# Kernel tuning notes

Hardware: AMD Instinct MI355X
Metric: run time of the kernel (lower is better)

## Reference

```python
import jax, jax.numpy as jnp
import numpy as np
from jax import lax

EPS = 1e-5


def _bn(x, gamma, beta, mean, var):
    # x: [B,C,H,W]; params: [C]
    inv = gamma / jnp.sqrt(var + EPS)
    return x * inv[None, :, None, None] + (beta - mean * inv)[None, :, None, None]


def _conv1x1(x, w):
    # w: [O, C] pointwise conv
    return jnp.einsum('oc,bchw->bohw', w, x)


def setup_inputs() -> dict:
    dim, num_heads = 256, 8
    B, H, W = 4, 40, 40
    key = jax.random.key(0)
    ks = jax.random.split(key, 12)
    inp = {
        'x': jax.random.normal(ks[0], (B, dim, H, W), jnp.float32),
        # qkv: Conv(dim, 2*dim, k=1) = conv1x1 (no bias) + BN + SiLU
        'qkv_w': jax.random.normal(ks[1], (2 * dim, dim), jnp.float32) * 0.05,
        'qkv_gamma': jax.random.uniform(ks[2], (2 * dim,), jnp.float32, 0.5, 1.5),
        'qkv_beta': jax.random.normal(ks[3], (2 * dim,), jnp.float32) * 0.05,
        'qkv_mean': jax.random.normal(ks[4], (2 * dim,), jnp.float32) * 0.05,
        'qkv_var': jax.random.uniform(ks[5], (2 * dim,), jnp.float32, 0.5, 1.5),
        # proj: Conv(dim, dim, k=1)
        'proj_w': jax.random.normal(ks[6], (dim, dim), jnp.float32) * 0.05,
        'proj_gamma': jax.random.uniform(ks[7], (dim,), jnp.float32, 0.5, 1.5),
        'proj_beta': jax.random.normal(ks[8], (dim,), jnp.float32) * 0.05,
        'proj_mean': jax.random.normal(ks[9], (dim,), jnp.float32) * 0.05,
        'proj_var': jax.random.uniform(ks[10], (dim,), jnp.float32, 0.5, 1.5),
        # pe: depthwise 3x3 conv (groups=dim, no bias) + BN (no activation)
        'pe_w': jax.random.normal(ks[11], (dim, 1, 3, 3), jnp.float32) * 0.1,
        'pe_gamma': jax.random.uniform(jax.random.fold_in(key, 100), (dim,), jnp.float32, 0.5, 1.5),
        'pe_beta': jax.random.normal(jax.random.fold_in(key, 101), (dim,), jnp.float32) * 0.05,
        'pe_mean': jax.random.normal(jax.random.fold_in(key, 102), (dim,), jnp.float32) * 0.05,
        'pe_var': jax.random.uniform(jax.random.fold_in(key, 103), (dim,), jnp.float32, 0.5, 1.5),
    }
    return inp


def reference(x, qkv_w, qkv_gamma, qkv_beta, qkv_mean, qkv_var,
              proj_w, proj_gamma, proj_beta, proj_mean, proj_var,
              pe_w, pe_gamma, pe_beta, pe_mean, pe_var):
    B, C, H, W = x.shape
    num_heads = 8
    head_dim = C // num_heads
    N = H * W

    # positional encoding: depthwise 3x3 conv + BN
    pe = lax.conv_general_dilated(
        x, pe_w, window_strides=(1, 1), padding='SAME',
        feature_group_count=C, dimension_numbers=('NCHW', 'OIHW', 'NCHW'))
    pe = _bn(pe, pe_gamma, pe_beta, pe_mean, pe_var)

    # qkv: 1x1 conv + BN + SiLU, then split into q, k along channels
    qkv = jax.nn.silu(_bn(_conv1x1(x, qkv_w), qkv_gamma, qkv_beta, qkv_mean, qkv_var))
    q, k = qkv[:, :C], qkv[:, C:]
    v = x + pe

    # reshape to heads: q,v -> [B,h,N,d]; k -> [B,h,d,N]
    q = q.reshape(B, num_heads, head_dim, N).transpose(0, 1, 3, 2)
    k = k.reshape(B, num_heads, head_dim, N)
    v = v.reshape(B, num_heads, head_dim, N).transpose(0, 1, 3, 2)

    scale = head_dim ** (-0.5)
    attn = jnp.einsum('bhnd,bhdm->bhnm', q, k) * scale  # [B,h,N,N]
    attn = jax.nn.softmax(attn, axis=-1)
    out = jnp.einsum('bhnm,bhmd->bhnd', attn, v)        # [B,h,N,d]
    out = out.transpose(0, 1, 3, 2).reshape(B, C, H, W)

    # proj: 1x1 conv + BN + SiLU
    return jax.nn.silu(_bn(_conv1x1(out, proj_w), proj_gamma, proj_beta, proj_mean, proj_var))
```

## Files before the change

### kernel.cpp

```cpp
#include <hip/hip_runtime.h>
#include <hip/hip_bf16.h>

typedef __attribute__((ext_vector_type(8))) short short8;
typedef __attribute__((ext_vector_type(4))) float f32x4;

__device__ __forceinline__ unsigned short f2bf(float f){
    union { float f; unsigned u; } uf; uf.f = f;
    unsigned u = uf.u;
    u += 0x7FFFu + ((u >> 16) & 1u);
    return (unsigned short)(u >> 16);
}
__device__ __forceinline__ int pack2(float a, float b){
    union { float f; unsigned u; } ua, ub; ua.f = a; ub.f = b;
    unsigned x = ua.u; x += 0x7FFFu + ((x >> 16) & 1u);
    unsigned y = ub.u; y += 0x7FFFu + ((y >> 16) & 1u);
    return (int)((x >> 16) | (y & 0xFFFF0000u));
}
__device__ __forceinline__ unsigned cvtpk(float lo, float hi){
    unsigned r;
    asm("v_cvt_pk_bf16_f32 %0, %1, %2" : "=v"(r) : "v"(lo), "v"(hi));
    return r;
}
__device__ __forceinline__ float fexp2(float x){
    return __builtin_amdgcn_exp2f(x);
}

#define N_SPATIAL 1600
#define QSCALE_LOG2E 0.25506601f
#define LSTR 40

__global__ __launch_bounds__(256) void k_head2(const float* __restrict__ x,
                                               const float* __restrict__ pw,
                                               const float* __restrict__ pg,
                                               const float* __restrict__ pb,
                                               const float* __restrict__ pm,
                                               const float* __restrict__ pv,
                                               unsigned short* __restrict__ x_t,
                                               unsigned short* __restrict__ v_mf){
    __shared__ float xs[32][163];
    int pbi = blockIdx.x;
    int b = pbi/200, h=(pbi/25)%8, kt=pbi%25;
    int t = threadIdx.x;
    int winStart = kt*64 - 48;
    const float* xbase = x + ((size_t)(b*256 + h*32))*N_SPATIAL;
    #pragma unroll
    for (int i=0;i<20;i++){
        int idx = t + i*256;
        int row = idx / 160, col = idx - row*160;
        int n = winStart + col;
        float val = ((unsigned)n < 1600u) ? xbase[(size_t)row*N_SPATIAL + n] : 0.f;
        xs[row][col] = val;
    }
    __syncthreads();

    {
        unsigned short* xtb = x_t + ((size_t)b*N_SPATIAL + kt*64)*256 + h*32;
        #pragma unroll
        for (int i=0;i<8;i++){
            int idx = t + i*256;
            int cl = idx & 31, nl = idx >> 5;
            xtb[(size_t)nl*256 + cl] = f2bf(xs[cl][nl + 48]);
        }
    }

    int f = t>>6, lane = t&63, ql = lane&15, lg = lane>>4;
    int d = (f>>1)*16 + ql;
    int c = h*32 + d;
    float inv = pg[c]*rsqrtf(pv[c]+1e-5f);
    float bias = pb[c]-pm[c]*inv;
    const float* w9 = pw + c*9;
    float w00=w9[0],w01=w9[1],w02=w9[2],w10=w9[3],w11=w9[4],w12=w9[5],w20=w9[6],w21=w9[7],w22=w9[8];
    const float* xr = xs[d];
    union { unsigned short u[8]; int4 i4; } vals;
    #pragma unroll
    for (int j=0;j<8;j++){
        int key = (f&1)*32 + (j>>2)*16 + 4*lg + (j&3);
        int n = kt*64 + key;
        int hh = n/40, ww = n - hh*40;
        int col = key + 48;
        float acc = 0.f;
        if (hh > 0){
            if (ww > 0)  acc += xr[col-41]*w00;
                         acc += xr[col-40]*w01;
            if (ww < 39) acc += xr[col-39]*w02;
        }
        if (ww > 0)  acc += xr[col-1]*w10;
                     acc += xr[col]*w11;
        if (ww < 39) acc += xr[col+1]*w12;
        if (hh < 39){
            if (ww > 0)  acc += xr[col+39]*w20;
                         acc += xr[col+40]*w21;
            if (ww < 39) acc += xr[col+41]*w22;
        }
        float out = xr[col] + acc*inv + bias;
        vals.u[j] = f2bf(out);
    }
    *reinterpret_cast<int4*>(v_mf + ((size_t)(pbi*4 + f)*64 + lane)*8) = vals.i4;
}

__global__ __launch_bounds__(256) void k_qkv2(const unsigned short* __restrict__ x_t,
                                              const float* __restrict__ wq,
                                              const float* __restrict__ g,
                                              const float* __restrict__ be,
                                              const float* __restrict__ mu,
                                              const float* __restrict__ va,
                                              unsigned short* __restrict__ qk_t){
    __shared__ alignas(16) unsigned short a_lds[64*LSTR];
    __shared__ alignas(16) unsigned short b_lds[64*LSTR];
    int bi = blockIdx.x;
    int b = bi / 200, ot = (bi/25) % 8, nt = bi % 25;
    int o0 = ot*64, n0 = nt*64;
    int tid = threadIdx.x, w = tid>>6, lane = tid&63;
    int row = tid>>2, col8 = (tid&3)*8;
    int ql = lane&15, lg = lane>>4;
    f32x4 acc[4];
    #pragma unroll
    for (int t=0;t<4;t++) acc[t] = (f32x4){0.f,0.f,0.f,0.f};
    const float* asrc = wq + (size_t)(o0+row)*256 + col8;
    const unsigned short* bsrc = x_t + ((size_t)b*N_SPATIAL + n0 + row)*256 + col8;
    for (int k0=0; k0<256; k0+=32){
        float4 f0 = *reinterpret_cast<const float4*>(asrc + k0);
        float4 f1 = *reinterpret_cast<const float4*>(asrc + k0 + 4);
        int4 av; av.x = pack2(f0.x,f0.y); av.y = pack2(f0.z,f0.w);
                 av.z = pack2(f1.x,f1.y); av.w = pack2(f1.z,f1.w);
        *reinterpret_cast<int4*>(&a_lds[row*LSTR + col8]) = av;
        *reinterpret_cast<int4*>(&b_lds[row*LSTR + col8]) = *reinterpret_cast<const int4*>(bsrc + k0);
        __syncthreads();
        short8 af = *reinterpret_cast<const short8*>(&a_lds[(16*w + ql)*LSTR + lg*8]);
        #pragma unroll
        for (int t=0;t<4;t++){
            short8 bf = *reinterpret_cast<const short8*>(&b_lds[(16*t + ql)*LSTR + lg*8]);
            acc[t] = __builtin_amdgcn_mfma_f32_16x16x32_bf16(af, bf, acc[t], 0, 0, 0);
        }
        __syncthreads();
    }
    int ob = o0 + 16*w + 4*lg;
    int grp = ob >> 5, d0 = ob & 31;
    float invr[4], b2r[4];
    #pragma unroll
    for (int r=0;r<4;r++){
        int o = ob + r;
        invr[r] = g[o] * rsqrtf(va[o] + 1e-5f);
        b2r[r]  = be[o] - mu[o]*invr[r];
    }
    float qs = (ob < 256) ? QSCALE_LOG2E : 1.0f;
    unsigned short* dstb = qk_t + ((size_t)(b*16 + grp)*N_SPATIAL)*32 + d0;
    #pragma unroll
    for (int t=0;t<4;t++){
        int n = n0 + 16*t + ql;
        float y[4];
        #pragma unroll
        for (int r=0;r<4;r++){
            float z = acc[t][r]*invr[r] + b2r[r];
            y[r] = (z / (1.f + __expf(-z))) * qs;
        }
        uint2 wv = make_uint2((unsigned)pack2(y[0],y[1]), (unsigned)pack2(y[2],y[3]));
        *reinterpret_cast<uint2*>(dstb + (size_t)n*32) = wv;
    }
}

__global__ __launch_bounds__(512) void k_attn7(const unsigned short* __restrict__ qk_t,
                                               const unsigned short* __restrict__ v_mf,
                                               unsigned short* __restrict__ ao_t){
    __shared__ alignas(16) unsigned short k_lds[3][64*40];
    __shared__ alignas(16) unsigned short v_lds[3][2048];
    int l = blockIdx.x;
    int xc = l & 7, j = l >> 3;
    int gg = xc + 8*(j/25);
    int bi = 25*gg + (j%25);
    int b = gg >> 3, h = gg & 7, qt = bi % 25;
    int tid = threadIdx.x, w = tid>>6, lane = tid&63;

    const unsigned short* ksrc = qk_t + ((size_t)(b*16+8+h)*N_SPATIAL)*32;
    const unsigned short* vms  = v_mf + (size_t)(b*200 + h*25)*2048;

    if (w < 4){
        int ql = lane&15, lg = lane>>4;
        int nq = qt*64 + w*16 + ql;
        const unsigned short* qsrc = qk_t + ((size_t)(b*16+h)*N_SPATIAL)*32;
        short8 qf = *reinterpret_cast<const short8*>(qsrc + (size_t)nq*32 + lg*8);
        f32x4 o0 = (f32x4){0.f,0.f,0.f,0.f};
        f32x4 o1 = (f32x4){0.f,0.f,0.f,0.f};
        float Sp = 0.f;

        asm volatile("" ::: "memory");
        __builtin_amdgcn_s_barrier();
        asm volatile("" ::: "memory");

        int cur = 0;
        for (int kt = 0; kt < 25; ++kt){
            const unsigned short* kb = &k_lds[cur][0];
            const unsigned short* vb = &v_lds[cur][0];
            short8 ka0 = *reinterpret_cast<const short8*>(kb + (size_t)( 0 + ql)*40 + lg*8);
            short8 ka1 = *reinterpret_cast<const short8*>(kb + (size_t)(16 + ql)*40 + lg*8);
            short8 ka2 = *reinterpret_cast<const short8*>(kb + (size_t)(32 + ql)*40 + lg*8);
            short8 ka3 = *reinterpret_cast<const short8*>(kb + (size_t)(48 + ql)*40 + lg*8);

            f32x4 z = (f32x4){0.f,0.f,0.f,0.f};
            f32x4 p0 = __builtin_amdgcn_mfma_f32_16x16x32_bf16(ka0, qf, z, 0,0,0);
            f32x4 p1 = __builtin_amdgcn_mfma_f32_16x16x32_bf16(ka1, qf, z, 0,0,0);
            f32x4 p2 = __builtin_amdgcn_mfma_f32_16x16x32_bf16(ka2, qf, z, 0,0,0);
            f32x4 p3 = __builtin_amdgcn_mfma_f32_16x16x32_bf16(ka3, qf, z, 0,0,0);

            #pragma unroll
            for (int r=0;r<4;r++){
                p0[r] = fexp2(p0[r]);
                p1[r] = fexp2(p1[r]);
                p2[r] = fexp2(p2[r]);
                p3[r] = fexp2(p3[r]);
            }
            Sp += ((p0[0]+p0[1])+(p0[2]+p0[3])) + ((p1[0]+p1[1])+(p1[2]+p1[3]))
                + ((p2[0]+p2[1])+(p2[2]+p2[3])) + ((p3[0]+p3[1])+(p3[2]+p3[3]));

            union { int4 i; short8 s8; } pb0, pb1;
            pb0.i = make_int4((int)cvtpk(p0[0],p0[1]), (int)cvtpk(p0[2],p0[3]),
                              (int)cvtpk(p1[0],p1[1]), (int)cvtpk(p1[2],p1[3]));
            pb1.i = make_int4((int)cvtpk(p2[0],p2[1]), (int)cvtpk(p2[2],p2[3]),
                              (int)cvtpk(p3[0],p3[1]), (int)cvtpk(p3[2],p3[3]));

            short8 va0 = *reinterpret_cast<const short8*>(vb +    0 + lane*8);
            short8 va1 = *reinterpret_cast<const short8*>(vb +  512 + lane*8);
            short8 va2 = *reinterpret_cast<const short8*>(vb + 1024 + lane*8);
            short8 va3 = *reinterpret_cast<const short8*>(vb + 1536 + lane*8);

            o0 = __builtin_amdgcn_mfma_f32_16x16x32_bf16(va0, pb0.s8, o0, 0,0,0);
            o0 = __builtin_amdgcn_mfma_f32_16x16x32_bf16(va1, pb1.s8, o0, 0,0,0);
            o1 = __builtin_amdgcn_mfma_f32_16x16x32_bf16(va2, pb0.s8, o1, 0,0,0);
            o1 = __builtin_amdgcn_mfma_f32_16x16x32_bf16(va3, pb1.s8, o1, 0,0,0);

            asm volatile("" ::: "memory");
            __builtin_amdgcn_s_barrier();
            asm volatile("" ::: "memory");
            cur = (cur==2) ? 0 : cur+1;
        }

        Sp += __shfl_xor(Sp, 16);
        Sp += __shfl_xor(Sp, 32);
        float inv = 1.f / Sp;
        size_t rowoff = ((size_t)b*N_SPATIAL + nq)*256 + h*32;
        uint2 w0 = make_uint2((unsigned)pack2(o0[0]*inv, o0[1]*inv),
                              (unsigned)pack2(o0[2]*inv, o0[3]*inv));
        *reinterpret_cast<uint2*>(ao_t + rowoff + 4*lg) = w0;
        uint2 w1 = make_uint2((unsigned)pack2(o1[0]*inv, o1[1]*inv),
                              (unsigned)pack2(o1[2]*inv, o1[3]*inv));
        *reinterpret_cast<uint2*>(ao_t + rowoff + 16 + 4*lg) = w1;
    } else {
        int pi = tid & 255;
        const unsigned short* kg = ksrc + pi*8;
        const unsigned short* vg = vms  + pi*8;
        unsigned short* kd = &k_lds[0][0] + (pi>>2)*40 + (pi&3)*8;
        unsigned short* vd = &v_lds[0][0] + pi*8;

        int4 a0 = *reinterpret_cast<const int4*>(kg);
        int4 b0 = *reinterpret_cast<const int4*>(vg);
        *reinterpret_cast<int4*>(kd) = a0;
        *reinterpret_cast<int4*>(vd) = b0;
        int4 a1 = *reinterpret_cast<const int4*>(kg + 2048);
        int4 b1 = *reinterpret_cast<const int4*>(vg + 2048);
        *reinterpret_cast<int4*>(kd + 2560) = a1;
        *reinterpret_cast<int4*>(vd + 2048) = b1;
        int4 hk = *reinterpret_cast<const int4*>(kg + 4096);
        int4 hv = *reinterpret_cast<const int4*>(vg + 4096);
        asm volatile("s_waitcnt lgkmcnt(0)" ::: "memory");
        __builtin_amdgcn_s_barrier();
        asm volatile("" ::: "memory");

        int wb = 2;
        for (int kt = 0; kt < 25; ++kt){
            if (kt < 23){
                *reinterpret_cast<int4*>(kd + wb*2560) = hk;
                *reinterpret_cast<int4*>(vd + wb*2048) = hv;
            }
            if (kt < 22){
                hk = *reinterpret_cast<const int4*>(kg + (size_t)(kt+3)*2048);
                hv = *reinterpret_cast<const int4*>(vg + (size_t)(kt+3)*2048);
            }
            asm volatile("s_waitcnt lgkmcnt(0)" ::: "memory");
            __builtin_amdgcn_s_barrier();
            asm volatile("" ::: "memory");
            wb = (wb==2) ? 0 : wb+1;
        }
    }
}

__global__ __launch_bounds__(256) void k_proj4(const unsigned short* __restrict__ ao_t,
                                               const float* __restrict__ wp,
                                               const float* __restrict__ g,
                                               const float* __restrict__ be,
                                               const float* __restrict__ mu,
                                               const float* __restrict__ va,
                                               float* __restrict__ out){
    __shared__ alignas(16) unsigned short a_lds[64*LSTR];
    __shared__ alignas(16) unsigned short b_lds[32*LSTR];
    int bi = blockIdx.x;
    int b = bi / 200, ot = (bi/50) % 4, nt = bi % 50;
    int o0 = ot*64, n0 = nt*32;
    int tid = threadIdx.x, w = tid>>6, lane = tid&63;
    int arow = tid>>2, acol8 = (tid&3)*8;
    int brow = tid>>3, bcol4 = (tid&7)*4;
    int ql = lane&15, lg = lane>>4;
    f32x4 acc[2];
    acc[0] = (f32x4){0.f,0.f,0.f,0.f};
    acc[1] = (f32x4){0.f,0.f,0.f,0.f};
    const float* asrc = wp + (size_t)(o0+arow)*256 + acol8;
    const unsigned short* bsrc = ao_t + ((size_t)b*N_SPATIAL + n0 + brow)*256 + bcol4;
    for (int k0=0; k0<256; k0+=32){
        float4 f0 = *reinterpret_cast<const float4*>(asrc + k0);
        float4 f1 = *reinterpret_cast<const float4*>(asrc + k0 + 4);
        int4 av; av.x = pack2(f0.x,f0.y); av.y = pack2(f0.z,f0.w);
                 av.z = pack2(f1.x,f1.y); av.w = pack2(f1.z,f1.w);
        *reinterpret_cast<int4*>(&a_lds[arow*LSTR + acol8]) = av;
        *reinterpret_cast<uint2*>(&b_lds[brow*LSTR + bcol4]) = *reinterpret_cast<const uint2*>(bsrc + k0);
        __syncthreads();
        short8 af = *reinterpret_cast<const short8*>(&a_lds[(16*w + ql)*LSTR + lg*8]);
        #pragma unroll
        for (int t=0;t<2;t++){
            short8 bf = *reinterpret_cast<const short8*>(&b_lds[(16*t + ql)*LSTR + lg*8]);
            acc[t] = __builtin_amdgcn_mfma_f32_16x16x32_bf16(af, bf, acc[t], 0, 0, 0);
        }
        __syncthreads();
    }
    #pragma unroll
    for (int r=0;r<4;r++){
        int o = o0 + 16*w + lg*4 + r;
        float inv = g[o] * rsqrtf(va[o] + 1e-5f);
        float b2  = be[o] - mu[o]*inv;
        float* dst = out + ((size_t)(b*256 + o))*N_SPATIAL;
        #pragma unroll
        for (int t=0;t<2;t++){
            int n = n0 + 16*t + ql;
            float z = acc[t][r]*inv + b2;
            float y = z / (1.f + __expf(-z));
            dst[n] = y;
        }
    }
}

extern "C" void kernel_launch(void* const* d_in, const int* in_sizes, int n_in,
                              void* d_out, int out_size, void* d_ws, size_t ws_size,
                              hipStream_t stream) {
    const float* x      = (const float*)d_in[0];
    const float* qkv_w  = (const float*)d_in[1];
    const float* qkv_g  = (const float*)d_in[2];
    const float* qkv_b  = (const float*)d_in[3];
    const float* qkv_m  = (const float*)d_in[4];
    const float* qkv_v  = (const float*)d_in[5];
    const float* proj_w = (const float*)d_in[6];
    const float* proj_g = (const float*)d_in[7];
    const float* proj_b = (const float*)d_in[8];
    const float* proj_m = (const float*)d_in[9];
    const float* proj_v = (const float*)d_in[10];
    const float* pe_w   = (const float*)d_in[11];
    const float* pe_g   = (const float*)d_in[12];
    const float* pe_b   = (const float*)d_in[13];
    const float* pe_m   = (const float*)d_in[14];
    const float* pe_v   = (const float*)d_in[15];

    char* ws = (char*)d_ws;
    unsigned short* x_t  = (unsigned short*)(ws);
    unsigned short* v_mf = (unsigned short*)(ws + 3276800);
    unsigned short* qk_t = (unsigned short*)(ws + 6553600);
    unsigned short* ao_t = (unsigned short*)(ws + 13107200);
    float* outp = (float*)d_out;

    k_head2<<<800, 256, 0, stream>>>(x, pe_w, pe_g, pe_b, pe_m, pe_v, x_t, v_mf);
    k_qkv2 <<<800, 256, 0, stream>>>(x_t, qkv_w, qkv_g, qkv_b, qkv_m, qkv_v, qk_t);
    k_attn7<<<800, 512, 0, stream>>>(qk_t, v_mf, ao_t);
    k_proj4<<<800, 256, 0, stream>>>(ao_t, proj_w, proj_g, proj_b, proj_m, proj_v, outp);
}
```

Baseline: 59.96 us.

## Process two key tiles per barrier in attention with double-buffered LDS pairs

The attention kernel now handles two 64-key tiles per loop step, cutting the number of block-wide barriers roughly in half. A triple buffer of single tiles becomes a double buffer of tile pairs, and the producer waves prefetch two tiles ahead into registers. Compute waves raise their scheduling priority around the MFMA and exp work. This costs more registers and LDS, and the odd final tile needs a special path.

```diff
diff --git a/kernel.cpp b/kernel.cpp
--- a/kernel.cpp
+++ b/kernel.cpp
@@ -159,16 +159,15 @@
     }
 }
 
-__global__ __launch_bounds__(512) void k_attn7(const unsigned short* __restrict__ qk_t,
+__global__ __launch_bounds__(512) void k_attn9(const unsigned short* __restrict__ qk_t,
                                                const unsigned short* __restrict__ v_mf,
                                                unsigned short* __restrict__ ao_t){
-    __shared__ alignas(16) unsigned short k_lds[3][64*40];
-    __shared__ alignas(16) unsigned short v_lds[3][2048];
+    __shared__ alignas(16) unsigned short k_lds[2][2*2560];
+    __shared__ alignas(16) unsigned short v_lds[2][2*2048];
     int l = blockIdx.x;
     int xc = l & 7, j = l >> 3;
     int gg = xc + 8*(j/25);
-    int bi = 25*gg + (j%25);
-    int b = gg >> 3, h = gg & 7, qt = bi % 25;
+    int b = gg >> 3, h = gg & 7, qt = j % 25;
     int tid = threadIdx.x, w = tid>>6, lane = tid&63;
 
     const unsigned short* ksrc = qk_t + ((size_t)(b*16+8+h)*N_SPATIAL)*32;
@@ -187,51 +186,92 @@
         __builtin_amdgcn_s_barrier();
         asm volatile("" ::: "memory");
 
-        int cur = 0;
-        for (int kt = 0; kt < 25; ++kt){
-            const unsigned short* kb = &k_lds[cur][0];
-            const unsigned short* vb = &v_lds[cur][0];
-            short8 ka0 = *reinterpret_cast<const short8*>(kb + (size_t)( 0 + ql)*40 + lg*8);
-            short8 ka1 = *reinterpret_cast<const short8*>(kb + (size_t)(16 + ql)*40 + lg*8);
-            short8 ka2 = *reinterpret_cast<const short8*>(kb + (size_t)(32 + ql)*40 + lg*8);
-            short8 ka3 = *reinterpret_cast<const short8*>(kb + (size_t)(48 + ql)*40 + lg*8);
+        for (int iv = 0; iv < 13; ++iv){
+            bool pair2 = (iv < 12);
+            const unsigned short* kb = &k_lds[iv&1][0];
+            const unsigned short* vb = &v_lds[iv&1][0];
+
+            __builtin_amdgcn_s_setprio(1);
+            short8 a0 = *reinterpret_cast<const short8*>(kb + (size_t)( 0 + ql)*40 + lg*8);
+            short8 a1 = *reinterpret_cast<const short8*>(kb + (size_t)(16 + ql)*40 + lg*8);
+            short8 a2 = *reinterpret_cast<const short8*>(kb + (size_t)(32 + ql)*40 + lg*8);
+            short8 a3 = *reinterpret_cast<const short8*>(kb + (size_t)(48 + ql)*40 + lg*8);
+            short8 c0, c1, c2, c3;
+            if (pair2){
+                const unsigned short* kb1 = kb + 2560;
+                c0 = *reinterpret_cast<const short8*>(kb1 + (size_t)( 0 + ql)*40 + lg*8);
+                c1 = *reinterpret_cast<const short8*>(kb1 + (size_t)(16 + ql)*40 + lg*8);
+                c2 = *reinterpret_cast<const short8*>(kb1 + (size_t)(32 + ql)*40 + lg*8);
+                c3 = *reinterpret_cast<const short8*>(kb1 + (size_t)(48 + ql)*40 + lg*8);
+            }
 
             f32x4 z = (f32x4){0.f,0.f,0.f,0.f};
-            f32x4 p0 = __builtin_amdgcn_mfma_f32_16x16x32_bf16(ka0, qf, z, 0,0,0);
-            f32x4 p1 = __builtin_amdgcn_mfma_f32_16x16x32_bf16(ka1, qf, z, 0,0,0);
-            f32x4 p2 = __builtin_amdgcn_mfma_f32_16x16x32_bf16(ka2, qf, z, 0,0,0);
-            f32x4 p3 = __builtin_amdgcn_mfma_f32_16x16x32_bf16(ka3, qf, z, 0,0,0);
+            f32x4 pA0 = __builtin_amdgcn_mfma_f32_16x16x32_bf16(a0, qf, z, 0,0,0);
+            f32x4 pA1 = __builtin_amdgcn_mfma_f32_16x16x32_bf16(a1, qf, z, 0,0,0);
+            f32x4 pA2 = __builtin_amdgcn_mfma_f32_16x16x32_bf16(a2, qf, z, 0,0,0);
+            f32x4 pA3 = __builtin_amdgcn_mfma_f32_16x16x32_bf16(a3, qf, z, 0,0,0);
+            f32x4 pB0, pB1, pB2, pB3;
+            if (pair2){
+                pB0 = __builtin_amdgcn_mfma_f32_16x16x32_bf16(c0, qf, z, 0,0,0);
+                pB1 = __builtin_amdgcn_mfma_f32_16x16x32_bf16(c1, qf, z, 0,0,0);
+                pB2 = __builtin_amdgcn_mfma_f32_16x16x32_bf16(c2, qf, z, 0,0,0);
+                pB3 = __builtin_amdgcn_mfma_f32_16x16x32_bf16(c3, qf, z, 0,0,0);
+            }
 
             #pragma unroll
             for (int r=0;r<4;r++){
-                p0[r] = fexp2(p0[r]);
-                p1[r] = fexp2(p1[r]);
-                p2[r] = fexp2(p2[r]);
-                p3[r] = fexp2(p3[r]);
-            }
-            Sp += ((p0[0]+p0[1])+(p0[2]+p0[3])) + ((p1[0]+p1[1])+(p1[2]+p1[3]))
-                + ((p2[0]+p2[1])+(p2[2]+p2[3])) + ((p3[0]+p3[1])+(p3[2]+p3[3]));
-
-            union { int4 i; short8 s8; } pb0, pb1;
-            pb0.i = make_int4((int)cvtpk(p0[0],p0[1]), (int)cvtpk(p0[2],p0[3]),
-                              (int)cvtpk(p1[0],p1[1]), (int)cvtpk(p1[2],p1[3]));
-            pb1.i = make_int4((int)cvtpk(p2[0],p2[1]), (int)cvtpk(p2[2],p2[3]),
-                              (int)cvtpk(p3[0],p3[1]), (int)cvtpk(p3[2],p3[3]));
-
-            short8 va0 = *reinterpret_cast<const short8*>(vb +    0 + lane*8);
-            short8 va1 = *reinterpret_cast<const short8*>(vb +  512 + lane*8);
-            short8 va2 = *reinterpret_cast<const short8*>(vb + 1024 + lane*8);
-            short8 va3 = *reinterpret_cast<const short8*>(vb + 1536 + lane*8);
-
-            o0 = __builtin_amdgcn_mfma_f32_16x16x32_bf16(va0, pb0.s8, o0, 0,0,0);
-            o0 = __builtin_amdgcn_mfma_f32_16x16x32_bf16(va1, pb1.s8, o0, 0,0,0);
-            o1 = __builtin_amdgcn_mfma_f32_16x16x32_bf16(va2, pb0.s8, o1, 0,0,0);
-            o1 = __builtin_amdgcn_mfma_f32_16x16x32_bf16(va3, pb1.s8, o1, 0,0,0);
+                pA0[r] = fexp2(pA0[r]);
+                pA1[r] = fexp2(pA1[r]);
+                pA2[r] = fexp2(pA2[r]);
+                pA3[r] = fexp2(pA3[r]);
+            }
+            Sp += ((pA0[0]+pA0[1])+(pA0[2]+pA0[3])) + ((pA1[0]+pA1[1])+(pA1[2]+pA1[3]))
+                + ((pA2[0]+pA2[1])+(pA2[2]+pA2[3])) + ((pA3[0]+pA3[1])+(pA3[2]+pA3[3]));
+            union { int4 i; short8 s8; } qa0, qa1;
+            qa0.i = make_int4((int)cvtpk(pA0[0],pA0[1]), (int)cvtpk(pA0[2],pA0[3]),
+                              (int)cvtpk(pA1[0],pA1[1]), (int)cvtpk(pA1[2],pA1[3]));
+            qa1.i = make_int4((int)cvtpk(pA2[0],pA2[1]), (int)cvtpk(pA2[2],pA2[3]),
+                              (int)cvtpk(pA3[0],pA3[1]), (int)cvtpk(pA3[2],pA3[3]));
+            {
+                short8 v0 = *reinterpret_cast<const short8*>(vb +    0 + lane*8);
+                short8 v1 = *reinterpret_cast<const short8*>(vb +  512 + lane*8);
+                short8 v2 = *reinterpret_cast<const short8*>(vb + 1024 + lane*8);
+                short8 v3 = *reinterpret_cast<const short8*>(vb + 1536 + lane*8);
+                o0 = __builtin_amdgcn_mfma_f32_16x16x32_bf16(v0, qa0.s8, o0, 0,0,0);
+                o0 = __builtin_amdgcn_mfma_f32_16x16x32_bf16(v1, qa1.s8, o0, 0,0,0);
+                o1 = __builtin_amdgcn_mfma_f32_16x16x32_bf16(v2, qa0.s8, o1, 0,0,0);
+                o1 = __builtin_amdgcn_mfma_f32_16x16x32_bf16(v3, qa1.s8, o1, 0,0,0);
+            }
+            if (pair2){
+                #pragma unroll
+                for (int r=0;r<4;r++){
+                    pB0[r] = fexp2(pB0[r]);
+                    pB1[r] = fexp2(pB1[r]);
+                    pB2[r] = fexp2(pB2[r]);
+                    pB3[r] = fexp2(pB3[r]);
+                }
+                Sp += ((pB0[0]+pB0[1])+(pB0[2]+pB0[3])) + ((pB1[0]+pB1[1])+(pB1[2]+pB1[3]))
+                    + ((pB2[0]+pB2[1])+(pB2[2]+pB2[3])) + ((pB3[0]+pB3[1])+(pB3[2]+pB3[3]));
+                union { int4 i; short8 s8; } qb0, qb1;
+                qb0.i = make_int4((int)cvtpk(pB0[0],pB0[1]), (int)cvtpk(pB0[2],pB0[3]),
+                                  (int)cvtpk(pB1[0],pB1[1]), (int)cvtpk(pB1[2],pB1[3]));
+                qb1.i = make_int4((int)cvtpk(pB2[0],pB2[1]), (int)cvtpk(pB2[2],pB2[3]),
+                                  (int)cvtpk(pB3[0],pB3[1]), (int)cvtpk(pB3[2],pB3[3]));
+                const unsigned short* vb1 = vb + 2048;
+                short8 v0 = *reinterpret_cast<const short8*>(vb1 +    0 + lane*8);
+                short8 v1 = *reinterpret_cast<const short8*>(vb1 +  512 + lane*8);
+                short8 v2 = *reinterpret_cast<const short8*>(vb1 + 1024 + lane*8);
+                short8 v3 = *reinterpret_cast<const short8*>(vb1 + 1536 + lane*8);
+                o0 = __builtin_amdgcn_mfma_f32_16x16x32_bf16(v0, qb0.s8, o0, 0,0,0);
+                o0 = __builtin_amdgcn_mfma_f32_16x16x32_bf16(v1, qb1.s8, o0, 0,0,0);
+                o1 = __builtin_amdgcn_mfma_f32_16x16x32_bf16(v2, qb0.s8, o1, 0,0,0);
+                o1 = __builtin_amdgcn_mfma_f32_16x16x32_bf16(v3, qb1.s8, o1, 0,0,0);
+            }
+            __builtin_amdgcn_s_setprio(0);
 
             asm volatile("" ::: "memory");
             __builtin_amdgcn_s_barrier();
             asm volatile("" ::: "memory");
-            cur = (cur==2) ? 0 : cur+1;
         }
 
         Sp += __shfl_xor(Sp, 16);
@@ -251,34 +291,48 @@
         unsigned short* kd = &k_lds[0][0] + (pi>>2)*40 + (pi&3)*8;
         unsigned short* vd = &v_lds[0][0] + pi*8;
 
-        int4 a0 = *reinterpret_cast<const int4*>(kg);
-        int4 b0 = *reinterpret_cast<const int4*>(vg);
-        *reinterpret_cast<int4*>(kd) = a0;
-        *reinterpret_cast<int4*>(vd) = b0;
-        int4 a1 = *reinterpret_cast<const int4*>(kg + 2048);
-        int4 b1 = *reinterpret_cast<const int4*>(vg + 2048);
-        *reinterpret_cast<int4*>(kd + 2560) = a1;
-        *reinterpret_cast<int4*>(vd + 2048) = b1;
-        int4 hk = *reinterpret_cast<const int4*>(kg + 4096);
-        int4 hv = *reinterpret_cast<const int4*>(vg + 4096);
+        {
+            int4 k0 = *reinterpret_cast<const int4*>(kg);
+            int4 k1 = *reinterpret_cast<const int4*>(kg + 2048);
+            int4 v0 = *reinterpret_cast<const int4*>(vg);
+            int4 v1 = *reinterpret_cast<const int4*>(vg + 2048);
+            *reinterpret_cast<int4*>(kd) = k0;
+            *reinterpret_cast<int4*>(kd + 2560) = k1;
+            *reinterpret_cast<int4*>(vd) = v0;
+            *reinterpret_cast<int4*>(vd + 2048) = v1;
+        }
+        int4 hk0 = *reinterpret_cast<const int4*>(kg + 2*2048);
+        int4 hk1 = *reinterpret_cast<const int4*>(kg + 3*2048);
+        int4 hv0 = *reinterpret_cast<const int4*>(vg + 2*2048);
+        int4 hv1 = *reinterpret_cast<const int4*>(vg + 3*2048);
         asm volatile("s_waitcnt lgkmcnt(0)" ::: "memory");
         __builtin_amdgcn_s_barrier();
         asm volatile("" ::: "memory");
 
-        int wb = 2;
-        for (int kt = 0; kt < 25; ++kt){
-            if (kt < 23){
-                *reinterpret_cast<int4*>(kd + wb*2560) = hk;
-                *reinterpret_cast<int4*>(vd + wb*2048) = hv;
-            }
-            if (kt < 22){
-                hk = *reinterpret_cast<const int4*>(kg + (size_t)(kt+3)*2048);
-                hv = *reinterpret_cast<const int4*>(vg + (size_t)(kt+3)*2048);
+        for (int iv = 0; iv < 13; ++iv){
+            if (iv < 12){
+                int wb = (iv+1)&1;
+                unsigned short* kdw = kd + (size_t)wb*2*2560;
+                unsigned short* vdw = vd + (size_t)wb*2*2048;
+                *reinterpret_cast<int4*>(kdw) = hk0;
+                *reinterpret_cast<int4*>(vdw) = hv0;
+                if (2*(iv+1)+1 < 25){
+                    *reinterpret_cast<int4*>(kdw + 2560) = hk1;
+                    *reinterpret_cast<int4*>(vdw + 2048) = hv1;
+                }
+                if (iv+2 <= 12){
+                    int t0 = 2*(iv+2);
+                    hk0 = *reinterpret_cast<const int4*>(kg + (size_t)t0*2048);
+                    hv0 = *reinterpret_cast<const int4*>(vg + (size_t)t0*2048);
+                    if (t0+1 < 25){
+                        hk1 = *reinterpret_cast<const int4*>(kg + (size_t)(t0+1)*2048);
+                        hv1 = *reinterpret_cast<const int4*>(vg + (size_t)(t0+1)*2048);
+                    }
+                }
             }
             asm volatile("s_waitcnt lgkmcnt(0)" ::: "memory");
             __builtin_amdgcn_s_barrier();
             asm volatile("" ::: "memory");
-            wb = (wb==2) ? 0 : wb+1;
         }
     }
 }
@@ -365,6 +419,6 @@
 
     k_head2<<<800, 256, 0, stream>>>(x, pe_w, pe_g, pe_b, pe_m, pe_v, x_t, v_mf);
     k_qkv2 <<<800, 256, 0, stream>>>(x_t, qkv_w, qkv_g, qkv_b, qkv_m, qkv_v, qk_t);
-    k_attn7<<<800, 512, 0, stream>>>(qk_t, v_mf, ao_t);
+    k_attn9<<<800, 512, 0, stream>>>(qk_t, v_mf, ao_t);
     k_proj4<<<800, 256, 0, stream>>>(ao_t, proj_w, proj_g, proj_b, proj_m, proj_v, outp);
 }
```

New measurement: 61.24 us. 2.1% more time.
